# Optimization experiments

Hardware: AMD Instinct MI355X
Metric: run time of the kernel (lower is better)

The kernel has to match this reference:

```python
import jax, jax.numpy as jnp
import numpy as np

V = 100000   # nodes
E = 3200000  # edges (avg degree 32)
K = 16       # radial filters
T = 4        # atom types


def setup_inputs() -> dict:
    key = jax.random.key(0)
    k1, k2, k3, k4 = jax.random.split(key, 4)
    feat = jax.random.randint(k1, (V, 1), 0, T).astype(jnp.float32)  # atomic-type ids as floats
    distances = jax.random.uniform(k2, (E, 1), jnp.float32) * 12.0   # pairwise distances in [0, 12)
    src = jax.random.randint(k3, (E,), 0, V, dtype=jnp.int32)
    dst = jax.random.randint(k4, (E,), 0, V, dtype=jnp.int32)
    interaction_cutoffs = jnp.full((K,), 12.0, dtype=jnp.float32)
    rbf_kernel_means = jnp.linspace(0.0, 12.0, K).astype(jnp.float32)
    rbf_kernel_scaling = jnp.ones((K,), dtype=jnp.float32)
    features_to_use = jnp.arange(T, dtype=jnp.float32)
    return {
        'feat': feat, 'distances': distances, 'src': src, 'dst': dst,
        'interaction_cutoffs': interaction_cutoffs,
        'rbf_kernel_means': rbf_kernel_means,
        'rbf_kernel_scaling': rbf_kernel_scaling,
        'features_to_use': features_to_use,
    }


def reference(feat, distances, src, dst, interaction_cutoffs,
              rbf_kernel_means, rbf_kernel_scaling, features_to_use):
    d = distances                                    # (E, 1)
    # RadialPooling: rbf * cosine cutoff, broadcast (E,1) vs (K,) -> (E,K)
    rbf = jnp.exp(-rbf_kernel_scaling * (d - rbf_kernel_means) ** 2)
    cos_v = 0.5 * (jnp.cos(jnp.pi * d / interaction_cutoffs) + 1.0)
    he = rbf * jnp.where(d <= interaction_cutoffs, cos_v, jnp.zeros_like(cos_v))  # (E, K)
    # one-hot atom-type features (V, T)
    hv = (feat == features_to_use[None, :]).astype(distances.dtype)
    # gather src features, outer product with radial features -> (E, T, K)
    msg = hv[src][:, :, None] * he[:, None, :]
    # scatter-sum to destination nodes -> (V, T*K)
    out = jax.ops.segment_sum(msg.reshape(msg.shape[0], -1), dst, num_segments=V)
    return out
```

## Files before the change

kernel.cpp:

```cpp
#include <hip/hip_runtime.h>
#include <math.h>

#define NV 100000
#define NE 3200000
#define NK 16
#define NT 4
#define NB 1563
#define NKEY 256
#define SCH 4096
#define NCHUNK ((NE + SCH - 1) / SCH)
#define NG8 8
#define CAPG8 384
#define NG1 1
#define CAPG1 2432
#define PI_F 3.14159265358979323846f
#define LOG2E_F 1.4426950408889634f


__global__ __launch_bounds__(256) void zero_out_kernel(float4* __restrict__ out, int n4) {
    int i = blockIdx.x * blockDim.x + threadIdx.x;
    if (i < n4) out[i] = make_float4(0.f, 0.f, 0.f, 0.f);
}

__global__ __launch_bounds__(256) void atomic_conv_edge_kernel(
    const float* __restrict__ feat, const float* __restrict__ dist,
    const int* __restrict__ src, const int* __restrict__ dst,
    const float* __restrict__ cutoffs, const float* __restrict__ means,
    const float* __restrict__ scaling, const float* __restrict__ feats_use,
    float* __restrict__ out)
{
    int e = blockIdx.x * blockDim.x + threadIdx.x;
    if (e >= NE) return;
    float d = dist[e];
    int s = src[e];
    int v = dst[e];
    float fv = feat[s];
    int ty = 0;
#pragma unroll
    for (int t = 1; t < NT; ++t) if (fv == feats_use[t]) ty = t;
    float* o = out + (size_t)v * (NT * NK) + (size_t)ty * NK;
#pragma unroll
    for (int k = 0; k < NK; ++k) {
        float c = cutoffs[k], m = means[k], sc = scaling[k];
        float dm = d - m;
        float rbf = __expf(-sc * dm * dm);
        float cosv = 0.5f * (__cosf(PI_F * d / c) + 1.0f);
        float he = (d <= c) ? rbf * cosv : 0.0f;
        __hip_atomic_fetch_add(o + k, he, __ATOMIC_RELAXED, __HIP_MEMORY_SCOPE_AGENT);
    }
}



template<int NG, int CAPG>
__global__ __launch_bounds__(256, 5) void scatter_kernel_t(
    const float* __restrict__ feat, const float* __restrict__ dist,
    const int* __restrict__ src, const int* __restrict__ dst,
    const float* __restrict__ feats_use,
    int* __restrict__ cursors, unsigned* __restrict__ payload)
{
    __shared__ unsigned pld[SCH];
    __shared__ int hist[NB];
    __shared__ int base[NB];

    int t = threadIdx.x;
    int g = blockIdx.x & (NG - 1);
    int chunkBase = blockIdx.x * SCH;
    int n = NE - chunkBase;
    if (n > SCH) n = SCH;

    float f1 = feats_use[1], f2 = feats_use[2], f3 = feats_use[3];

    for (int i = t; i < NB; i += 256) hist[i] = 0;
    __syncthreads();

    int nq = n >> 2;
    const float4* d4 = (const float4*)(dist + chunkBase);
    const int4*   s4 = (const int4*)(src + chunkBase);
    const int4*   v4 = (const int4*)(dst + chunkBase);
    for (int i = t; i < nq; i += 256) {
        float4 dd = d4[i];
        int4 ss = s4[i];
        int4 vv = v4[i];
        float dv[4] = {dd.x, dd.y, dd.z, dd.w};
        int   sv[4] = {ss.x, ss.y, ss.z, ss.w};
        int   vb[4] = {vv.x, vv.y, vv.z, vv.w};
#pragma unroll
        for (int j = 0; j < 4; ++j) {
            float fv = feat[sv[j]];
            int v = vb[j];
            int ty = (fv == f1) ? 1 : (fv == f2) ? 2 : (fv == f3) ? 3 : 0;
            unsigned packed = (__float_as_uint(dv[j]) & 0xFFFFFE00u) |
                              ((unsigned)ty << 7) | (unsigned)(v & 63);
            pld[4 * i + j] = packed;
            atomicAdd(&hist[v >> 6], 1);
        }
    }
    for (int i = (nq << 2) + t; i < n; i += 256) {
        int e = chunkBase + i;
        float d = dist[e];
        float fv = feat[src[e]];
        int v = dst[e];
        int ty = (fv == f1) ? 1 : (fv == f2) ? 2 : (fv == f3) ? 3 : 0;
        pld[i] = (__float_as_uint(d) & 0xFFFFFE00u) |
                 ((unsigned)ty << 7) | (unsigned)(v & 63);
        atomicAdd(&hist[v >> 6], 1);
    }
    __syncthreads();

    for (int i = t; i < NB; i += 256) {
        int c = hist[i];
        if (c) base[i] = __hip_atomic_fetch_add(&cursors[i * NG + g], c,
                                                __ATOMIC_RELAXED, __HIP_MEMORY_SCOPE_AGENT);
        hist[i] = 0;
    }
    __syncthreads();

    for (int i = t; i < nq; i += 256) {
        int4 vv = v4[i];
        int vb[4] = {vv.x, vv.y, vv.z, vv.w};
#pragma unroll
        for (int j = 0; j < 4; ++j) {
            int b = vb[j] >> 6;
            int lp = atomicAdd(&hist[b], 1);
            int idx = base[b] + lp;
            if (idx < CAPG)
                payload[((size_t)b * NG + g) * CAPG + idx] = pld[4 * i + j];
        }
    }
    for (int i = (nq << 2) + t; i < n; i += 256) {
        int b = dst[chunkBase + i] >> 6;
        int lp = atomicAdd(&hist[b], 1);
        int idx = base[b] + lp;
        if (idx < CAPG)
            payload[((size_t)b * NG + g) * CAPG + idx] = pld[i];
    }
}

#define RUN_SEG(i0, i1, ACC)                                    \
    _Pragma("unroll 2")                                         \
    for (int i = (i0); i < (i1); ++i) {                         \
        unsigned p = srt[i];                                    \
        float d = __uint_as_float(p & 0xFFFFFE00u);             \
        float cv = 0.5f * (__cosf(w0 * d) + 1.0f);              \
        cv = (d <= c0) ? cv : 0.0f;                             \
        float dm = d - m0;                                      \
        float tt = c1 * dm * dm;                                \
        float uu = fmaf(um, dm, uc);                            \
        _Pragma("unroll")                                       \
        for (int k = 0; k < NK; ++k) {                          \
            float e = exp2f(tt);                                \
            ACC[k] = fmaf(e, cv, ACC[k]);                       \
            tt += uu;                                           \
            uu += du;                                           \
        }                                                       \
    }

#define RUN_SEG_GEN(i0, i1, ACC)                                \
    for (int i = (i0); i < (i1); ++i) {                         \
        unsigned p = srt[i];                                    \
        float d = __uint_as_float(p & 0xFFFFFE00u);             \
        _Pragma("unroll")                                       \
        for (int k = 0; k < NK; ++k) {                          \
            float c = cutoffs[k], m = means[k], sc = scaling[k];\
            float dmm = d - m;                                  \
            float rbf = __expf(-sc * dmm * dmm);                \
            float cosv = 0.5f * (__cosf(PI_F * d / c) + 1.0f);  \
            float he = (d <= c) ? rbf * cosv : 0.0f;            \
            ACC[k] += he;                                       \
        }                                                       \
    }

template<int NG, int CAPG>
__global__ __launch_bounds__(256, 6) void reduce_kernel_t(
    const unsigned* __restrict__ payload, const int* __restrict__ counts,
    const float* __restrict__ cutoffs, const float* __restrict__ means,
    const float* __restrict__ scaling, float* __restrict__ out)
{
    __shared__ unsigned srt[NG * CAPG];
    __shared__ int scn[NKEY];
    __shared__ int cur[NKEY];
    __shared__ int coff[NKEY + 1];

    int b = blockIdx.x;
    int t = threadIdx.x;
    const unsigned* __restrict__ pay = payload + (size_t)b * NG * CAPG;

    int cnt[NG];
#pragma unroll
    for (int g = 0; g < NG; ++g) {
        int c = counts[b * NG + g];
        cnt[g] = (c > CAPG) ? CAPG : c;
    }

    float m0 = means[0], s0v = scaling[0], c0 = cutoffs[0];
    float delta = means[1] - m0;
    bool uniform = true;
#pragma unroll
    for (int k = 0; k < NK; ++k) {
        uniform = uniform && (scaling[k] == s0v) && (cutoffs[k] == c0)
                  && (fabsf(means[k] - (m0 + (float)k * delta)) <= 1e-3f);
    }
    float w0 = PI_F / c0;
    float c1 = -s0v * LOG2E_F;
    float um = -2.0f * c1 * delta;
    float uc = c1 * delta * delta;
    float du = 2.0f * uc;

    scn[t] = 0;
    __syncthreads();
#pragma unroll
    for (int g = 0; g < NG; ++g) {
        const unsigned* __restrict__ pg = pay + g * CAPG;
        for (int i = t; i < cnt[g]; i += 256) {
            unsigned p = pg[i];
            atomicAdd(&scn[((p & 63) << 2) | ((p >> 7) & 3)], 1);
        }
    }
    __syncthreads();

    int x = scn[t];
#pragma unroll
    for (int off = 1; off < 256; off <<= 1) {
        int v = (t >= off) ? scn[t - off] : 0;
        __syncthreads();
        scn[t] += v;
        __syncthreads();
    }
    int excl = scn[t] - x;
    coff[t] = excl;
    cur[t] = excl;
    if (t == 255) coff[NKEY] = scn[255];
    __syncthreads();

#pragma unroll
    for (int g = 0; g < NG; ++g) {
        const unsigned* __restrict__ pg = pay + g * CAPG;
        for (int i = t; i < cnt[g]; i += 256) {
            unsigned p = pg[i];
            int pos = atomicAdd(&cur[((p & 63) << 2) | ((p >> 7) & 3)], 1);
            srt[pos] = p;
        }
    }
    __syncthreads();

    float acc[NK];
#pragma unroll
    for (int k = 0; k < NK; ++k) acc[k] = 0.f;

    int e0 = coff[t];
    int e1 = coff[t + 1];

    if (uniform) {
        RUN_SEG(e0, e1, acc)
    } else {
        RUN_SEG_GEN(e0, e1, acc)
    }

    int node = b * 64 + (t >> 2);
    if (node < NV) {
        float4* o = (float4*)(out + (size_t)node * 64 + (size_t)(t & 3) * 16);
#pragma unroll
        for (int k = 0; k < 4; ++k)
            o[k] = make_float4(acc[4 * k], acc[4 * k + 1], acc[4 * k + 2], acc[4 * k + 3]);
    }
}

extern "C" void kernel_launch(void* const* d_in, const int* in_sizes, int n_in,
                              void* d_out, int out_size, void* d_ws, size_t ws_size,
                              hipStream_t stream) {
    const float* feat      = (const float*)d_in[0];
    const float* dist      = (const float*)d_in[1];
    const int*   src       = (const int*)d_in[2];
    const int*   dst       = (const int*)d_in[3];
    const float* cutoffs   = (const float*)d_in[4];
    const float* means     = (const float*)d_in[5];
    const float* scaling   = (const float*)d_in[6];
    const float* feats_use = (const float*)d_in[7];
    float* out = (float*)d_out;

    auto plan = [](int ng, int capg, size_t& o_cursors, size_t& o_payload) {
        size_t off = 0;
        auto alloc = [&](size_t bytes) {
            size_t cur = off;
            off = (off + bytes + 255) & ~(size_t)255;
            return cur;
        };
        o_cursors = alloc((size_t)NB * ng * 4);
        o_payload = alloc((size_t)NB * ng * capg * 4);
        return off;
    };

    size_t oc8, op8, oc1, op1;
    size_t need8 = plan(NG8, CAPG8, oc8, op8);
    size_t need1 = plan(NG1, CAPG1, oc1, op1);

    char* ws = (char*)d_ws;
    if (ws_size >= need8) {
        int* cursors = (int*)(ws + oc8);
        unsigned* payload = (unsigned*)(ws + op8);
        hipMemsetAsync(cursors, 0, (size_t)NB * NG8 * 4, stream);
        scatter_kernel_t<NG8, CAPG8><<<NCHUNK, 256, 0, stream>>>(
            feat, dist, src, dst, feats_use, cursors, payload);
        reduce_kernel_t<NG8, CAPG8><<<NB, 256, 0, stream>>>(
            payload, cursors, cutoffs, means, scaling, out);
    } else if (ws_size >= need1) {
        int* cursors = (int*)(ws + oc1);
        unsigned* payload = (unsigned*)(ws + op1);
        hipMemsetAsync(cursors, 0, (size_t)NB * NG1 * 4, stream);
        scatter_kernel_t<NG1, CAPG1><<<NCHUNK, 256, 0, stream>>>(
            feat, dist, src, dst, feats_use, cursors, payload);
        reduce_kernel_t<NG1, CAPG1><<<NB, 256, 0, stream>>>(
            payload, cursors, cutoffs, means, scaling, out);
    } else {
        int n4 = out_size / 4;
        zero_out_kernel<<<(n4 + 255) / 256, 256, 0, stream>>>((float4*)out, n4);
        atomic_conv_edge_kernel<<<(NE + 255) / 256, 256, 0, stream>>>(
            feat, dist, src, dst, cutoffs, means, scaling, feats_use, out);
    }
}
```

Before: 208.5 us.

## Replace global atomic cursors with per-chunk local bucket sort and offsets

The scatter kernel now sorts each edge chunk locally by destination bucket and writes the payload contiguously, along with a per-chunk prefix-offset table, so it no longer needs global atomic cursors or a memset. The reduce kernel gathers each bucket's segments from all chunks with per-thread copy loops into shared memory before the existing type/node sort. Both block scans now use wavefront shuffles, and streaming loads and stores are marked nontemporal. The trade-off is that each reduce block must read many small scattered segments (about 782 chunks, roughly 2 edges each), which can hurt memory coalescing.

```diff
diff --git a/kernel.cpp b/kernel.cpp
--- a/kernel.cpp
+++ b/kernel.cpp
@@ -6,15 +6,17 @@
 #define NK 16
 #define NT 4
 #define NB 1563
+#define NBP 1564
 #define NKEY 256
 #define SCH 4096
 #define NCHUNK ((NE + SCH - 1) / SCH)
-#define NG8 8
-#define CAPG8 384
-#define NG1 1
-#define CAPG1 2432
+#define RCAP 2432
+#define CPT 7
 #define PI_F 3.14159265358979323846f
 #define LOG2E_F 1.4426950408889634f
+
+typedef float vfloat4 __attribute__((ext_vector_type(4)));
+typedef int   vint4   __attribute__((ext_vector_type(4)));
 
 
 __global__ __launch_bounds__(256) void zero_out_kernel(float4* __restrict__ out, int n4) {
@@ -52,20 +54,20 @@
 
 
 
-template<int NG, int CAPG>
-__global__ __launch_bounds__(256, 5) void scatter_kernel_t(
+__global__ __launch_bounds__(256, 5) void scatter_kernel(
     const float* __restrict__ feat, const float* __restrict__ dist,
     const int* __restrict__ src, const int* __restrict__ dst,
     const float* __restrict__ feats_use,
-    int* __restrict__ cursors, unsigned* __restrict__ payload)
+    unsigned short* __restrict__ offs, unsigned* __restrict__ payload)
 {
     __shared__ unsigned pld[SCH];
+    __shared__ unsigned short bkt[SCH];
     __shared__ int hist[NB];
-    __shared__ int base[NB];
+    __shared__ int wsum[4];
 
     int t = threadIdx.x;
-    int g = blockIdx.x & (NG - 1);
-    int chunkBase = blockIdx.x * SCH;
+    int c = blockIdx.x;
+    int chunkBase = c * SCH;
     int n = NE - chunkBase;
     if (n > SCH) n = SCH;
 
@@ -75,25 +77,23 @@
     __syncthreads();
 
     int nq = n >> 2;
-    const float4* d4 = (const float4*)(dist + chunkBase);
-    const int4*   s4 = (const int4*)(src + chunkBase);
-    const int4*   v4 = (const int4*)(dst + chunkBase);
+    const vfloat4* d4 = (const vfloat4*)(dist + chunkBase);
+    const vint4*   s4 = (const vint4*)(src + chunkBase);
+    const vint4*   v4 = (const vint4*)(dst + chunkBase);
     for (int i = t; i < nq; i += 256) {
-        float4 dd = d4[i];
-        int4 ss = s4[i];
-        int4 vv = v4[i];
-        float dv[4] = {dd.x, dd.y, dd.z, dd.w};
-        int   sv[4] = {ss.x, ss.y, ss.z, ss.w};
-        int   vb[4] = {vv.x, vv.y, vv.z, vv.w};
+        vfloat4 dd = __builtin_nontemporal_load(&d4[i]);
+        vint4   ss = __builtin_nontemporal_load(&s4[i]);
+        vint4   vv = __builtin_nontemporal_load(&v4[i]);
 #pragma unroll
         for (int j = 0; j < 4; ++j) {
-            float fv = feat[sv[j]];
-            int v = vb[j];
+            float fv = feat[ss[j]];
+            int v = vv[j];
             int ty = (fv == f1) ? 1 : (fv == f2) ? 2 : (fv == f3) ? 3 : 0;
-            unsigned packed = (__float_as_uint(dv[j]) & 0xFFFFFE00u) |
-                              ((unsigned)ty << 7) | (unsigned)(v & 63);
-            pld[4 * i + j] = packed;
-            atomicAdd(&hist[v >> 6], 1);
+            int b = v >> 6;
+            pld[4 * i + j] = (__float_as_uint(dd[j]) & 0xFFFFFE00u) |
+                             ((unsigned)ty << 7) | (unsigned)(v & 63);
+            bkt[4 * i + j] = (unsigned short)b;
+            atomicAdd(&hist[b], 1);
         }
     }
     for (int i = (nq << 2) + t; i < n; i += 256) {
@@ -102,38 +102,57 @@
         float fv = feat[src[e]];
         int v = dst[e];
         int ty = (fv == f1) ? 1 : (fv == f2) ? 2 : (fv == f3) ? 3 : 0;
+        int b = v >> 6;
         pld[i] = (__float_as_uint(d) & 0xFFFFFE00u) |
                  ((unsigned)ty << 7) | (unsigned)(v & 63);
-        atomicAdd(&hist[v >> 6], 1);
-    }
-    __syncthreads();
-
-    for (int i = t; i < NB; i += 256) {
-        int c = hist[i];
-        if (c) base[i] = __hip_atomic_fetch_add(&cursors[i * NG + g], c,
-                                                __ATOMIC_RELAXED, __HIP_MEMORY_SCOPE_AGENT);
-        hist[i] = 0;
-    }
-    __syncthreads();
-
-    for (int i = t; i < nq; i += 256) {
-        int4 vv = v4[i];
-        int vb[4] = {vv.x, vv.y, vv.z, vv.w};
-#pragma unroll
-        for (int j = 0; j < 4; ++j) {
-            int b = vb[j] >> 6;
-            int lp = atomicAdd(&hist[b], 1);
-            int idx = base[b] + lp;
-            if (idx < CAPG)
-                payload[((size_t)b * NG + g) * CAPG + idx] = pld[4 * i + j];
+        bkt[i] = (unsigned short)b;
+        atomicAdd(&hist[b], 1);
+    }
+    __syncthreads();
+
+    int base_i = t * CPT;
+    int loc[CPT];
+    int sum = 0;
+#pragma unroll
+    for (int i = 0; i < CPT; ++i) {
+        int idx = base_i + i;
+        int v = (idx < NB) ? hist[idx] : 0;
+        loc[i] = sum;
+        sum += v;
+    }
+    int lane = t & 63, wv = t >> 6;
+    int inc = sum;
+#pragma unroll
+    for (int o = 1; o < 64; o <<= 1) {
+        int u = __shfl_up(inc, o, 64);
+        if (lane >= o) inc += u;
+    }
+    if (lane == 63) wsum[wv] = inc;
+    __syncthreads();
+    int add = 0;
+#pragma unroll
+    for (int w = 0; w < 4; ++w) add += (w < wv) ? wsum[w] : 0;
+    int excl = add + inc - sum;
+
+    unsigned short* __restrict__ oc = offs + (size_t)c * NBP;
+#pragma unroll
+    for (int i = 0; i < CPT; ++i) {
+        int idx = base_i + i;
+        int pref = excl + loc[i];
+        if (idx < NB) {
+            oc[idx] = (unsigned short)pref;
+            hist[idx] = pref;
+        } else if (idx == NB) {
+            oc[NB] = (unsigned short)n;
         }
     }
-    for (int i = (nq << 2) + t; i < n; i += 256) {
-        int b = dst[chunkBase + i] >> 6;
-        int lp = atomicAdd(&hist[b], 1);
-        int idx = base[b] + lp;
-        if (idx < CAPG)
-            payload[((size_t)b * NG + g) * CAPG + idx] = pld[i];
+    __syncthreads();
+
+    unsigned* __restrict__ pout = payload + (size_t)chunkBase;
+    for (int i = t; i < n; i += 256) {
+        int b = bkt[i];
+        int pos = atomicAdd(&hist[b], 1);
+        pout[pos] = pld[i];
     }
 }
 
@@ -171,27 +190,21 @@
         }                                                       \
     }
 
-template<int NG, int CAPG>
-__global__ __launch_bounds__(256, 6) void reduce_kernel_t(
-    const unsigned* __restrict__ payload, const int* __restrict__ counts,
+__global__ __launch_bounds__(256, 7) void reduce_kernel(
+    const unsigned* __restrict__ payload, const unsigned short* __restrict__ offs,
     const float* __restrict__ cutoffs, const float* __restrict__ means,
     const float* __restrict__ scaling, float* __restrict__ out)
 {
-    __shared__ unsigned srt[NG * CAPG];
+    __shared__ unsigned raw[RCAP];
+    __shared__ unsigned srt[RCAP];
     __shared__ int scn[NKEY];
     __shared__ int cur[NKEY];
     __shared__ int coff[NKEY + 1];
+    __shared__ int wsum[4];
+    __shared__ int tot;
 
     int b = blockIdx.x;
     int t = threadIdx.x;
-    const unsigned* __restrict__ pay = payload + (size_t)b * NG * CAPG;
-
-    int cnt[NG];
-#pragma unroll
-    for (int g = 0; g < NG; ++g) {
-        int c = counts[b * NG + g];
-        cnt[g] = (c > CAPG) ? CAPG : c;
-    }
 
     float m0 = means[0], s0v = scaling[0], c0 = cutoffs[0];
     float delta = means[1] - m0;
@@ -208,39 +221,54 @@
     float du = 2.0f * uc;
 
     scn[t] = 0;
-    __syncthreads();
-#pragma unroll
-    for (int g = 0; g < NG; ++g) {
-        const unsigned* __restrict__ pg = pay + g * CAPG;
-        for (int i = t; i < cnt[g]; i += 256) {
-            unsigned p = pg[i];
-            atomicAdd(&scn[((p & 63) << 2) | ((p >> 7) & 3)], 1);
+    if (t == 0) tot = 0;
+    __syncthreads();
+
+    for (int c = t; c < NCHUNK; c += 256) {
+        const unsigned short* oc = offs + (size_t)c * NBP + b;
+        int s = oc[0];
+        int e = oc[1];
+        int cnt = e - s;
+        if (cnt > 0) {
+            int pos = atomicAdd(&tot, cnt);
+            if (pos + cnt > RCAP) cnt = (pos < RCAP) ? (RCAP - pos) : 0;
+            const unsigned* __restrict__ pp = payload + (size_t)c * SCH + s;
+            for (int j = 0; j < cnt; ++j) raw[pos + j] = pp[j];
         }
     }
     __syncthreads();
+    int n = tot;
+    if (n > RCAP) n = RCAP;
+
+    for (int i = t; i < n; i += 256) {
+        unsigned p = raw[i];
+        atomicAdd(&scn[((p & 63) << 2) | ((p >> 7) & 3)], 1);
+    }
+    __syncthreads();
 
     int x = scn[t];
-#pragma unroll
-    for (int off = 1; off < 256; off <<= 1) {
-        int v = (t >= off) ? scn[t - off] : 0;
-        __syncthreads();
-        scn[t] += v;
-        __syncthreads();
-    }
-    int excl = scn[t] - x;
+    int lane = t & 63, wv = t >> 6;
+    int inc = x;
+#pragma unroll
+    for (int o = 1; o < 64; o <<= 1) {
+        int u = __shfl_up(inc, o, 64);
+        if (lane >= o) inc += u;
+    }
+    if (lane == 63) wsum[wv] = inc;
+    __syncthreads();
+    int add = 0;
+#pragma unroll
+    for (int w = 0; w < 4; ++w) add += (w < wv) ? wsum[w] : 0;
+    int excl = add + inc - x;
     coff[t] = excl;
     cur[t] = excl;
-    if (t == 255) coff[NKEY] = scn[255];
-    __syncthreads();
-
-#pragma unroll
-    for (int g = 0; g < NG; ++g) {
-        const unsigned* __restrict__ pg = pay + g * CAPG;
-        for (int i = t; i < cnt[g]; i += 256) {
-            unsigned p = pg[i];
-            int pos = atomicAdd(&cur[((p & 63) << 2) | ((p >> 7) & 3)], 1);
-            srt[pos] = p;
-        }
+    if (t == 255) coff[NKEY] = n;
+    __syncthreads();
+
+    for (int i = t; i < n; i += 256) {
+        unsigned p = raw[i];
+        int pos = atomicAdd(&cur[((p & 63) << 2) | ((p >> 7) & 3)], 1);
+        srt[pos] = p;
     }
     __syncthreads();
 
@@ -259,10 +287,12 @@
 
     int node = b * 64 + (t >> 2);
     if (node < NV) {
-        float4* o = (float4*)(out + (size_t)node * 64 + (size_t)(t & 3) * 16);
-#pragma unroll
-        for (int k = 0; k < 4; ++k)
-            o[k] = make_float4(acc[4 * k], acc[4 * k + 1], acc[4 * k + 2], acc[4 * k + 3]);
+        vfloat4* o = (vfloat4*)(out + (size_t)node * 64 + (size_t)(t & 3) * 16);
+#pragma unroll
+        for (int k = 0; k < 4; ++k) {
+            vfloat4 v = {acc[4 * k], acc[4 * k + 1], acc[4 * k + 2], acc[4 * k + 3]};
+            __builtin_nontemporal_store(v, &o[k]);
+        }
     }
 }
 
@@ -279,43 +309,31 @@
     const float* feats_use = (const float*)d_in[7];
     float* out = (float*)d_out;
 
-    auto plan = [](int ng, int capg, size_t& o_cursors, size_t& o_payload) {
-        size_t off = 0;
-        auto alloc = [&](size_t bytes) {
-            size_t cur = off;
-            off = (off + bytes + 255) & ~(size_t)255;
-            return cur;
-        };
-        o_cursors = alloc((size_t)NB * ng * 4);
-        o_payload = alloc((size_t)NB * ng * capg * 4);
-        return off;
+    size_t off = 0;
+    auto alloc = [&](size_t bytes) {
+        size_t cur = off;
+        off = (off + bytes + 255) & ~(size_t)255;
+        return cur;
     };
-
-    size_t oc8, op8, oc1, op1;
-    size_t need8 = plan(NG8, CAPG8, oc8, op8);
-    size_t need1 = plan(NG1, CAPG1, oc1, op1);
-
-    char* ws = (char*)d_ws;
-    if (ws_size >= need8) {
-        int* cursors = (int*)(ws + oc8);
-        unsigned* payload = (unsigned*)(ws + op8);
-        hipMemsetAsync(cursors, 0, (size_t)NB * NG8 * 4, stream);
-        scatter_kernel_t<NG8, CAPG8><<<NCHUNK, 256, 0, stream>>>(
-            feat, dist, src, dst, feats_use, cursors, payload);
-        reduce_kernel_t<NG8, CAPG8><<<NB, 256, 0, stream>>>(
-            payload, cursors, cutoffs, means, scaling, out);
-    } else if (ws_size >= need1) {
-        int* cursors = (int*)(ws + oc1);
-        unsigned* payload = (unsigned*)(ws + op1);
-        hipMemsetAsync(cursors, 0, (size_t)NB * NG1 * 4, stream);
-        scatter_kernel_t<NG1, CAPG1><<<NCHUNK, 256, 0, stream>>>(
-            feat, dist, src, dst, feats_use, cursors, payload);
-        reduce_kernel_t<NG1, CAPG1><<<NB, 256, 0, stream>>>(
-            payload, cursors, cutoffs, means, scaling, out);
-    } else {
+    size_t o_offs    = alloc((size_t)NCHUNK * NBP * 2);
+    size_t o_payload = alloc((size_t)NCHUNK * SCH * 4);
+    size_t needed = off;
+
+    if (ws_size < needed) {
         int n4 = out_size / 4;
         zero_out_kernel<<<(n4 + 255) / 256, 256, 0, stream>>>((float4*)out, n4);
         atomic_conv_edge_kernel<<<(NE + 255) / 256, 256, 0, stream>>>(
             feat, dist, src, dst, cutoffs, means, scaling, feats_use, out);
-    }
-}
+        return;
+    }
+
+    char* ws = (char*)d_ws;
+    unsigned short* offs = (unsigned short*)(ws + o_offs);
+    unsigned* payload    = (unsigned*)(ws + o_payload);
+
+    scatter_kernel<<<NCHUNK, 256, 0, stream>>>(
+        feat, dist, src, dst, feats_use, offs, payload);
+
+    reduce_kernel<<<NB, 256, 0, stream>>>(
+        payload, offs, cutoffs, means, scaling, out);
+}
```

Result: faster. 191.5 us (-8.2%).
